# Kernel optimization log

Hardware: AMD Instinct MI355X
Metric: run time of the kernel (lower is better)

The kernel has to match this reference:

```python
import jax, jax.numpy as jnp
import numpy as np

TOP_K = 8
NUM_EXPERTS = 64
IN_FEATURES = 4096
TOKENS = 16384


def setup_inputs() -> dict:
    key = jax.random.key(0)
    kx, kw, kb = jax.random.split(key, 3)
    x = jax.random.normal(kx, (TOKENS, IN_FEATURES), dtype=jnp.float32)
    # nn.Linear(in_features, num_experts): W [E, D], b [E]
    bound = 1.0 / np.sqrt(IN_FEATURES)
    W = jax.random.uniform(kw, (NUM_EXPERTS, IN_FEATURES), dtype=jnp.float32, minval=-bound, maxval=bound)
    b = jax.random.uniform(kb, (NUM_EXPERTS,), dtype=jnp.float32, minval=-bound, maxval=bound)
    return {"x": x, "W": W, "b": b}


def reference(x, W, b):
    # gate logits: [T, E]
    logits = jnp.einsum('td,ed->te', x, W) + b
    scores = jax.nn.softmax(logits, axis=-1)
    # top-k per token: [T, K]
    vals, idx = jax.lax.top_k(scores, TOP_K)
    # faithful to torch.sum(expert_values): normalize by GLOBAL sum over all tokens
    weights = vals / jnp.sum(vals)
    return (idx.reshape(-1), weights)
```

## Files before the change

### kernel.cpp

```cpp
#include <hip/hip_runtime.h>
#include <math.h>

typedef float f4 __attribute__((ext_vector_type(4)));

#define TOKENS 16384
#define DIM    4096
#define NE     64
#define KTOP   8
#define BM     64
#define BK     32
#define NGRP   4
#define KRANGE (DIM / NGRP)
#define NTILE  (KRANGE / BK)
#define NT     256
#define NBLK   (TOKENS / BM)

__global__ __launch_bounds__(NT, 1) void gate_topk_kernel(
    const float* __restrict__ x, const float* __restrict__ W,
    const float* __restrict__ bias, float* __restrict__ idx_out,
    float* __restrict__ val_out, float* __restrict__ blocksums)
{
    __shared__ float smem[NGRP * 4096];
    __shared__ float bsum[NGRP];

    const int tid = threadIdx.x;
    const int g   = tid >> 6;
    const int t   = tid & 63;
    const int k4  = t & 7;
    const int m0  = t >> 3;
    const int tx  = t & 7;
    const int ty  = t >> 3;
    const int row0 = blockIdx.x * BM;

    float* As = &smem[g * 4096];
    float* Bs = As + 2048;

    const float* xa = x + (size_t)(row0 + m0) * DIM + (g * KRANGE) + (k4 << 2);
    const float* wb = W + (size_t)m0 * DIM + (g * KRANGE) + (k4 << 2);

    float acc[8][8] = {};
    f4 fa[8], fb[8];

#define LOAD(kt) do {                                                   \
        _Pragma("unroll")                                               \
        for (int s = 0; s < 8; ++s) {                                   \
            fa[s] = *(const f4*)(xa + (size_t)(s << 3) * DIM + (kt) * BK); \
            fb[s] = *(const f4*)(wb + (size_t)(s << 3) * DIM + (kt) * BK); \
        }                                                               \
    } while (0)

#define WRITE_TILE() do {                                               \
        const int wbase = (k4 << 8) + m0;                               \
        _Pragma("unroll")                                               \
        for (int s = 0; s < 8; ++s) {                                   \
            const int so = ((s ^ k4) << 3);                             \
            _Pragma("unroll")                                           \
            for (int j = 0; j < 4; ++j) {                               \
                As[wbase + (j << 6) + so] = fa[s][j];                   \
                Bs[wbase + (j << 6) + so] = fb[s][j];                   \
            }                                                           \
        }                                                               \
    } while (0)

#define COMPUTE() do {                                                  \
        _Pragma("unroll")                                               \
        for (int k2 = 0; k2 < 8; ++k2) {                                \
            const int ao = ((ty ^ k2) << 3);                            \
            const int bo = ((tx ^ k2) << 3);                            \
            _Pragma("unroll")                                           \
            for (int j2 = 0; j2 < 4; ++j2) {                            \
                const int base = (((k2 << 2) + j2) << 6);               \
                const f4 A0 = *(const f4*)&As[base + ao];               \
                const f4 A1 = *(const f4*)&As[base + ao + 4];           \
                const f4 B0 = *(const f4*)&Bs[base + bo];               \
                const f4 B1 = *(const f4*)&Bs[base + bo + 4];           \
                _Pragma("unroll")                                       \
                for (int i = 0; i < 4; ++i) {                           \
                    _Pragma("unroll")                                   \
                    for (int j = 0; j < 4; ++j) {                       \
                        acc[i][j]         = fmaf(A0[i], B0[j], acc[i][j]);         \
                        acc[i][j + 4]     = fmaf(A0[i], B1[j], acc[i][j + 4]);     \
                        acc[i + 4][j]     = fmaf(A1[i], B0[j], acc[i + 4][j]);     \
                        acc[i + 4][j + 4] = fmaf(A1[i], B1[j], acc[i + 4][j + 4]); \
                    }                                                   \
                }                                                       \
            }                                                           \
        }                                                               \
    } while (0)

    LOAD(0);
    WRITE_TILE();
    for (int kt = 0; kt < NTILE - 1; ++kt) {
        LOAD(kt + 1);
        COMPUTE();
        WRITE_TILE();
    }
    COMPUTE();

#undef LOAD
#undef WRITE_TILE
#undef COMPUTE

#pragma unroll
    for (int i = 0; i < 8; ++i) {
        const int pr = ((ty << 3) + i) << 6;
        f4 v0 = { acc[i][0], acc[i][1], acc[i][2], acc[i][3] };
        f4 v1 = { acc[i][4], acc[i][5], acc[i][6], acc[i][7] };
        *(f4*)&As[pr + (tx << 3)]     = v0;
        *(f4*)&As[pr + (tx << 3) + 4] = v1;
    }
    __syncthreads();

    const int lane = t;
    const float bv = bias[lane];
    float wsum = 0.0f;
#pragma unroll
    for (int tt = 0; tt < 16; ++tt) {
        const int tl = (g << 4) + tt;
        const int token = row0 + tl;
        const float logit = smem[0 * 4096 + tl * 64 + lane]
                          + smem[1 * 4096 + tl * 64 + lane]
                          + smem[2 * 4096 + tl * 64 + lane]
                          + smem[3 * 4096 + tl * 64 + lane] + bv;
        float mx = logit;
#pragma unroll
        for (int off = 32; off > 0; off >>= 1)
            mx = fmaxf(mx, __shfl_xor(mx, off, 64));
        const float p = expf(logit - mx);
        float s = p;
#pragma unroll
        for (int off = 32; off > 0; off >>= 1)
            s += __shfl_xor(s, off, 64);
        const float rs = 1.0f / s;
        float pv = p;
#pragma unroll
        for (int j = 0; j < KTOP; ++j) {
            float v = pv; int e = lane;
#pragma unroll
            for (int off = 1; off < 64; off <<= 1) {
                const float v2 = __shfl_xor(v, off, 64);
                const int   e2 = __shfl_xor(e, off, 64);
                if (v2 > v || (v2 == v && e2 < e)) { v = v2; e = e2; }
            }
            const float val = v * rs;
            if (lane == j) {
                idx_out[token * KTOP + j] = (float)e;
                val_out[token * KTOP + j] = val;
            }
            if (lane == e) pv = -1.0f;
            wsum += val;
        }
    }
    if (lane == 0) bsum[g] = wsum;
    __syncthreads();
    if (tid == 0)
        blocksums[blockIdx.x] = bsum[0] + bsum[1] + bsum[2] + bsum[3];
}

__global__ __launch_bounds__(256) void scale_kernel(
    const float* __restrict__ blocksums, float* __restrict__ vals)
{
    float total = 0.0f;
    for (int i = 0; i < NBLK; ++i) total += blocksums[i];
    const int i = blockIdx.x * blockDim.x + threadIdx.x;
    vals[i] = vals[i] / total;
}

extern "C" void kernel_launch(void* const* d_in, const int* in_sizes, int n_in,
                              void* d_out, int out_size, void* d_ws, size_t ws_size,
                              hipStream_t stream)
{
    const float* x = (const float*)d_in[0];
    const float* W = (const float*)d_in[1];
    const float* b = (const float*)d_in[2];
    float* idx_out = (float*)d_out;
    float* val_out = idx_out + (size_t)TOKENS * KTOP;
    float* blocksums = (float*)d_ws;

    gate_topk_kernel<<<NBLK, NT, 0, stream>>>(x, W, b, idx_out, val_out, blocksums);
    scale_kernel<<<(TOKENS * KTOP) / 256, 256, 0, stream>>>(blocksums, val_out);
}
```

Before: 214.8 us.

## Halve token tile per block, re-swizzle shared memory, vectorize blocksum reduction

Reduces the block tile from 64 to 32 tokens, doubling the grid to 512 blocks. It drops the one-block-per-CU launch bound so more waves can be resident to hide memory latency. Each thread now computes a 4x8 accumulator using a new rotation-based shared-memory swizzle, and the scale kernel reads block sums as float4. In exchange the expert weights are re-read by twice as many blocks, and each FMA needs more LDS reads.

Measured after the change: 255.6 us. 19.0% more time.

```diff
diff --git a/kernel.cpp b/kernel.cpp
--- a/kernel.cpp
+++ b/kernel.cpp
@@ -7,7 +7,7 @@
 #define DIM    4096
 #define NE     64
 #define KTOP   8
-#define BM     64
+#define BM     32
 #define BK     32
 #define NGRP   4
 #define KRANGE (DIM / NGRP)
@@ -15,77 +15,69 @@
 #define NT     256
 #define NBLK   (TOKENS / BM)
 
-__global__ __launch_bounds__(NT, 1) void gate_topk_kernel(
+__global__ __launch_bounds__(NT) void gate_topk_kernel(
     const float* __restrict__ x, const float* __restrict__ W,
     const float* __restrict__ bias, float* __restrict__ idx_out,
     float* __restrict__ val_out, float* __restrict__ blocksums)
 {
-    __shared__ float smem[NGRP * 4096];
+    __shared__ float smem[NGRP * 3072];
     __shared__ float bsum[NGRP];
 
     const int tid = threadIdx.x;
     const int g   = tid >> 6;
     const int t   = tid & 63;
     const int k4  = t & 7;
-    const int m0  = t >> 3;
-    const int tx  = t & 7;
-    const int ty  = t >> 3;
+    const int r   = t >> 3;
+    const int te  = t & 7;
+    const int tq  = t >> 3;
     const int row0 = blockIdx.x * BM;
 
-    float* As = &smem[g * 4096];
-    float* Bs = As + 2048;
+    float* As = &smem[g * 3072];
+    float* Bs = As + 1024;
 
-    const float* xa = x + (size_t)(row0 + m0) * DIM + (g * KRANGE) + (k4 << 2);
-    const float* wb = W + (size_t)m0 * DIM + (g * KRANGE) + (k4 << 2);
+    const float* xa = x + (size_t)(row0 + r) * DIM + g * KRANGE + (k4 << 2);
+    const float* wb = W + (size_t)r * DIM + g * KRANGE + (k4 << 2);
 
-    float acc[8][8] = {};
-    f4 fa[8], fb[8];
+    float acc[4][8] = {};
+    f4 fa[4], fb[8];
 
-#define LOAD(kt) do {                                                   \
-        _Pragma("unroll")                                               \
-        for (int s = 0; s < 8; ++s) {                                   \
+#define LOAD(kt) do {                                                    \
+        _Pragma("unroll")                                                \
+        for (int s = 0; s < 4; ++s)                                      \
             fa[s] = *(const f4*)(xa + (size_t)(s << 3) * DIM + (kt) * BK); \
+        _Pragma("unroll")                                                \
+        for (int s = 0; s < 8; ++s)                                      \
             fb[s] = *(const f4*)(wb + (size_t)(s << 3) * DIM + (kt) * BK); \
-        }                                                               \
     } while (0)
 
-#define WRITE_TILE() do {                                               \
-        const int wbase = (k4 << 8) + m0;                               \
-        _Pragma("unroll")                                               \
-        for (int s = 0; s < 8; ++s) {                                   \
-            const int so = ((s ^ k4) << 3);                             \
-            _Pragma("unroll")                                           \
-            for (int j = 0; j < 4; ++j) {                               \
-                As[wbase + (j << 6) + so] = fa[s][j];                   \
-                Bs[wbase + (j << 6) + so] = fb[s][j];                   \
-            }                                                           \
-        }                                                               \
+#define WRITE_TILE() do {                                                \
+        _Pragma("unroll")                                                \
+        for (int j = 0; j < 4; ++j) {                                    \
+            const int kk = (k4 << 2) + j;                                \
+            _Pragma("unroll")                                            \
+            for (int s = 0; s < 4; ++s)                                  \
+                As[kk * 32 + ((r + (s << 3) + (kk << 2)) & 31)] = fa[s][j]; \
+            _Pragma("unroll")                                            \
+            for (int s = 0; s < 8; ++s)                                  \
+                Bs[kk * 64 + ((r + (s << 3) + (kk << 2)) & 63)] = fb[s][j]; \
+        }                                                                \
     } while (0)
 
-#define COMPUTE() do {                                                  \
-        _Pragma("unroll")                                               \
-        for (int k2 = 0; k2 < 8; ++k2) {                                \
-            const int ao = ((ty ^ k2) << 3);                            \
-            const int bo = ((tx ^ k2) << 3);                            \
-            _Pragma("unroll")                                           \
-            for (int j2 = 0; j2 < 4; ++j2) {                            \
-                const int base = (((k2 << 2) + j2) << 6);               \
-                const f4 A0 = *(const f4*)&As[base + ao];               \
-                const f4 A1 = *(const f4*)&As[base + ao + 4];           \
-                const f4 B0 = *(const f4*)&Bs[base + bo];               \
-                const f4 B1 = *(const f4*)&Bs[base + bo + 4];           \
-                _Pragma("unroll")                                       \
-                for (int i = 0; i < 4; ++i) {                           \
-                    _Pragma("unroll")                                   \
-                    for (int j = 0; j < 4; ++j) {                       \
-                        acc[i][j]         = fmaf(A0[i], B0[j], acc[i][j]);         \
-                        acc[i][j + 4]     = fmaf(A0[i], B1[j], acc[i][j + 4]);     \
-                        acc[i + 4][j]     = fmaf(A1[i], B0[j], acc[i + 4][j]);     \
-                        acc[i + 4][j + 4] = fmaf(A1[i], B1[j], acc[i + 4][j + 4]); \
-                    }                                                   \
-                }                                                       \
-            }                                                           \
-        }                                                               \
+#define COMPUTE() do {                                                   \
+        _Pragma("unroll")                                                \
+        for (int kk = 0; kk < BK; ++kk) {                                \
+            const f4 A  = *(const f4*)&As[kk * 32 + (((tq + kk) << 2) & 31)]; \
+            const f4 B0 = *(const f4*)&Bs[kk * 64 + (((te << 3) + (kk << 2)) & 63)]; \
+            const f4 B1 = *(const f4*)&Bs[kk * 64 + (((te << 3) + 4 + (kk << 2)) & 63)]; \
+            _Pragma("unroll")                                            \
+            for (int i = 0; i < 4; ++i) {                                \
+                _Pragma("unroll")                                        \
+                for (int j = 0; j < 4; ++j) {                            \
+                    acc[i][j]     = fmaf(A[i], B0[j], acc[i][j]);        \
+                    acc[i][j + 4] = fmaf(A[i], B1[j], acc[i][j + 4]);    \
+                }                                                        \
+            }                                                            \
+        }                                                                \
     } while (0)
 
     LOAD(0);
@@ -102,12 +94,12 @@
 #undef COMPUTE
 
 #pragma unroll
-    for (int i = 0; i < 8; ++i) {
-        const int pr = ((ty << 3) + i) << 6;
+    for (int i = 0; i < 4; ++i) {
+        const int pr = ((tq << 2) + i) << 6;
         f4 v0 = { acc[i][0], acc[i][1], acc[i][2], acc[i][3] };
         f4 v1 = { acc[i][4], acc[i][5], acc[i][6], acc[i][7] };
-        *(f4*)&As[pr + (tx << 3)]     = v0;
-        *(f4*)&As[pr + (tx << 3) + 4] = v1;
+        *(f4*)&As[pr + (te << 3)]     = v0;
+        *(f4*)&As[pr + (te << 3) + 4] = v1;
     }
     __syncthreads();
 
@@ -115,13 +107,13 @@
     const float bv = bias[lane];
     float wsum = 0.0f;
 #pragma unroll
-    for (int tt = 0; tt < 16; ++tt) {
-        const int tl = (g << 4) + tt;
+    for (int tt = 0; tt < 8; ++tt) {
+        const int tl = (g << 3) + tt;
         const int token = row0 + tl;
-        const float logit = smem[0 * 4096 + tl * 64 + lane]
-                          + smem[1 * 4096 + tl * 64 + lane]
-                          + smem[2 * 4096 + tl * 64 + lane]
-                          + smem[3 * 4096 + tl * 64 + lane] + bv;
+        const float logit = smem[0 * 3072 + tl * 64 + lane]
+                          + smem[1 * 3072 + tl * 64 + lane]
+                          + smem[2 * 3072 + tl * 64 + lane]
+                          + smem[3 * 3072 + tl * 64 + lane] + bv;
         float mx = logit;
 #pragma unroll
         for (int off = 32; off > 0; off >>= 1)
@@ -161,7 +153,10 @@
     const float* __restrict__ blocksums, float* __restrict__ vals)
 {
     float total = 0.0f;
-    for (int i = 0; i < NBLK; ++i) total += blocksums[i];
+    for (int i = 0; i < NBLK / 4; ++i) {
+        const f4 v = *(const f4*)(blocksums + i * 4);
+        total += v[0] + v[1] + v[2] + v[3];
+    }
     const int i = blockIdx.x * blockDim.x + threadIdx.x;
     vals[i] = vals[i] / total;
 }
```
